# Kernel tuning notes

Hardware: AMD Instinct MI355X
Metric: run time of the kernel (lower is better)

The kernel has to match this reference:

```python
import jax, jax.numpy as jnp
import numpy as np

D_MODEL = 2048
N_HEADS = 16
D_K = D_MODEL // N_HEADS


def setup_inputs() -> dict:
    key = jax.random.key(0)
    k1, k2, k3 = jax.random.split(key, 3)
    x = jax.random.normal(k1, (2, 2048, D_MODEL), dtype=jnp.float32)
    # torch Linear convention: weight [out_features, in_features], y = x @ W.T
    W_qkv = jax.random.normal(k2, (3 * D_MODEL, D_MODEL), dtype=jnp.float32) * (D_MODEL ** -0.5)
    W_out = jax.random.normal(k3, (D_MODEL, D_MODEL), dtype=jnp.float32) * (D_MODEL ** -0.5)
    return {"x": x, "W_qkv": W_qkv, "W_out": W_out}


def reference(x, W_qkv, W_out):
    batch, seq_len, d_model = x.shape
    qkv = jnp.einsum('bsd,ed->bse', x, W_qkv)  # [B,S,3*D]
    qkv = qkv.reshape(batch, seq_len, 3, N_HEADS, D_K)
    qkv = jnp.transpose(qkv, (2, 0, 3, 1, 4))  # [3,B,H,S,Dk]
    Q, K, V = qkv[0], qkv[1], qkv[2]
    scores = jnp.einsum('bhqd,bhkd->bhqk', Q, K) / jnp.sqrt(jnp.float32(D_K))
    causal_mask = jnp.triu(jnp.ones((seq_len, seq_len), dtype=bool), k=1)
    scores = jnp.where(causal_mask, jnp.float32(-jnp.inf), scores)
    attn = jax.nn.softmax(scores, axis=-1)
    out = jnp.einsum('bhqk,bhkd->bhqd', attn, V)  # [B,H,S,Dk]
    out = jnp.transpose(out, (0, 2, 1, 3)).reshape(batch, seq_len, d_model)
    return jnp.einsum('bsd,ed->bse', out, W_out)
```

## Files before the change

### kernel.cpp

```cpp
#include <hip/hip_runtime.h>
#include <hip/hip_bf16.h>


typedef short bf16x8 __attribute__((ext_vector_type(8)));
typedef float f32x4  __attribute__((ext_vector_type(4)));

#define MFMA(a, b, c) __builtin_amdgcn_mfma_f32_16x16x32_bf16((a), (b), (c), 0, 0, 0)

#define GLDS16(gp, lp) __builtin_amdgcn_global_load_lds(                        \
    (const __attribute__((address_space(1))) void*)(gp),                        \
    (__attribute__((address_space(3))) void*)(lp), 16, 0, 0)

static __device__ __forceinline__ unsigned short f2bf(float f) {
    __hip_bfloat16 h = __float2bfloat16(f);
    return *reinterpret_cast<unsigned short*>(&h);
}

__global__ __launch_bounds__(256) void cvt3_f32_bf16(const float* __restrict__ x,
                                                     const float* __restrict__ wq,
                                                     const float* __restrict__ wo,
                                                     unsigned short* __restrict__ xb,
                                                     unsigned short* __restrict__ wqb,
                                                     unsigned short* __restrict__ wob) {
    const int i = blockIdx.x * 256 + threadIdx.x;
    const float* src; unsigned short* dst; int k;
    if (i < 2097152)      { src = x;  dst = xb;  k = i; }
    else if (i < 5242880) { src = wq; dst = wqb; k = i - 2097152; }
    else                  { src = wo; dst = wob; k = i - 5242880; }
    float4 v = reinterpret_cast<const float4*>(src)[k];
    ushort4 o;
    o.x = f2bf(v.x); o.y = f2bf(v.y); o.z = f2bf(v.z); o.w = f2bf(v.w);
    reinterpret_cast<ushort4*>(dst)[k] = o;
}

template <bool BF16OUT>
__global__ __launch_bounds__(256) void gemm_bt64(const unsigned short* __restrict__ A,
                                                 const unsigned short* __restrict__ W,
                                                 void* __restrict__ Cout,
                                                 int M, int N, int K) {
    __shared__ unsigned short As[128 * 64];
    __shared__ unsigned short Bs[128 * 64];
    const int tid = threadIdx.x;
    const int w = tid >> 6, lane = tid & 63;
    const int fr = lane & 15, fq = lane >> 4;
    const int m0 = blockIdx.y * 128, n0 = blockIdx.x * 128;
    const int wr = w >> 1, wc = w & 1;

    f32x4 acc[4][4];
#pragma unroll
    for (int a = 0; a < 4; a++)
#pragma unroll
        for (int b = 0; b < 4; b++) acc[a][b] = f32x4{0.f, 0.f, 0.f, 0.f};

    const int srow = lane >> 3;
    const int sce  = ((lane & 7) ^ (lane >> 3)) * 8;

    for (int kt = 0; kt < K; kt += 64) {
        __syncthreads();
#pragma unroll
        for (int q = 0; q < 4; ++q) {
            const int i = w * 4 + q;
            const int r = i * 8 + srow;
            GLDS16(A + (size_t)(m0 + r) * K + kt + sce, As + i * 512);
            GLDS16(W + (size_t)(n0 + r) * K + kt + sce, Bs + i * 512);
        }
        asm volatile("s_waitcnt vmcnt(0)" ::: "memory");
        __syncthreads();

#pragma unroll
        for (int kk = 0; kk < 2; ++kk) {
            bf16x8 af[4], bfr[4];
#pragma unroll
            for (int mi = 0; mi < 4; mi++) {
                const int row = wr * 64 + mi * 16 + fr;
                af[mi] = *reinterpret_cast<const bf16x8*>(
                    As + row * 64 + ((((kk * 64 + fq * 16) ^ ((fr & 7) << 4))) >> 1));
            }
#pragma unroll
            for (int ni = 0; ni < 4; ni++) {
                const int row = wc * 64 + ni * 16 + fr;
                bfr[ni] = *reinterpret_cast<const bf16x8*>(
                    Bs + row * 64 + ((((kk * 64 + fq * 16) ^ ((fr & 7) << 4))) >> 1));
            }
            __builtin_amdgcn_s_setprio(1);
#pragma unroll
            for (int mi = 0; mi < 4; mi++)
#pragma unroll
                for (int ni = 0; ni < 4; ni++)
                    acc[mi][ni] = MFMA(af[mi], bfr[ni], acc[mi][ni]);
            __builtin_amdgcn_s_setprio(0);
        }
    }

#pragma unroll
    for (int mi = 0; mi < 4; mi++) {
#pragma unroll
        for (int i = 0; i < 4; i++) {
            const int row = m0 + wr * 64 + mi * 16 + fq * 4 + i;
            const size_t base = (size_t)row * N + n0 + wc * 64 + fr;
#pragma unroll
            for (int ni = 0; ni < 4; ni++) {
                if (BF16OUT)
                    ((unsigned short*)Cout)[base + ni * 16] = f2bf(acc[mi][ni][i]);
                else
                    ((float*)Cout)[base + ni * 16] = acc[mi][ni][i];
            }
        }
    }
}

template <bool BF16OUT>
__global__ __launch_bounds__(256) void gemm_bt64_db(const unsigned short* __restrict__ A,
                                                    const unsigned short* __restrict__ W,
                                                    void* __restrict__ Cout,
                                                    int M, int N, int K) {
    __shared__ unsigned short As[2][128 * 64];
    __shared__ unsigned short Bs[2][128 * 64];
    const int tid = threadIdx.x;
    const int w = tid >> 6, lane = tid & 63;
    const int fr = lane & 15, fq = lane >> 4;
    const int m0 = blockIdx.y * 128, n0 = blockIdx.x * 128;
    const int wr = w >> 1, wc = w & 1;

    f32x4 acc[4][4];
#pragma unroll
    for (int a = 0; a < 4; a++)
#pragma unroll
        for (int b = 0; b < 4; b++) acc[a][b] = f32x4{0.f, 0.f, 0.f, 0.f};

    const int srow = lane >> 3;
    const int sce  = ((lane & 7) ^ (lane >> 3)) * 8;

    auto stage = [&](int kt, int bufi) {
#pragma unroll
        for (int q = 0; q < 4; ++q) {
            const int i = w * 4 + q;
            const int r = i * 8 + srow;
            GLDS16(A + (size_t)(m0 + r) * K + kt + sce, &As[bufi][i * 512]);
            GLDS16(W + (size_t)(n0 + r) * K + kt + sce, &Bs[bufi][i * 512]);
        }
    };

    const int NT = K >> 6;
    int cur = 0;
    stage(0, 0);
    __syncthreads();

    for (int it = 0; it < NT; ++it) {
        if (it + 1 < NT) stage((it + 1) << 6, cur ^ 1);
#pragma unroll
        for (int kk = 0; kk < 2; ++kk) {
            bf16x8 af[4], bfr[4];
#pragma unroll
            for (int mi = 0; mi < 4; mi++) {
                const int row = wr * 64 + mi * 16 + fr;
                af[mi] = *reinterpret_cast<const bf16x8*>(
                    &As[cur][0] + row * 64 + ((((kk * 64 + fq * 16) ^ ((fr & 7) << 4))) >> 1));
            }
#pragma unroll
            for (int ni = 0; ni < 4; ni++) {
                const int row = wc * 64 + ni * 16 + fr;
                bfr[ni] = *reinterpret_cast<const bf16x8*>(
                    &Bs[cur][0] + row * 64 + ((((kk * 64 + fq * 16) ^ ((fr & 7) << 4))) >> 1));
            }
            __builtin_amdgcn_s_setprio(1);
#pragma unroll
            for (int mi = 0; mi < 4; mi++)
#pragma unroll
                for (int ni = 0; ni < 4; ni++)
                    acc[mi][ni] = MFMA(af[mi], bfr[ni], acc[mi][ni]);
            __builtin_amdgcn_s_setprio(0);
        }
        __syncthreads();
        cur ^= 1;
    }

#pragma unroll
    for (int mi = 0; mi < 4; mi++) {
#pragma unroll
        for (int i = 0; i < 4; i++) {
            const int row = m0 + wr * 64 + mi * 16 + fq * 4 + i;
            const size_t base = (size_t)row * N + n0 + wc * 64 + fr;
#pragma unroll
            for (int ni = 0; ni < 4; ni++) {
                if (BF16OUT)
                    ((unsigned short*)Cout)[base + ni * 16] = f2bf(acc[mi][ni][i]);
                else
                    ((float*)Cout)[base + ni * 16] = acc[mi][ni][i];
            }
        }
    }
}

__global__ __launch_bounds__(256) void transpose_v(const unsigned short* __restrict__ qkv,
                                                   unsigned short* __restrict__ vT) {
    __shared__ unsigned short t[32][33];
    const int b = blockIdx.z, ts = blockIdx.x, tu = blockIdx.y;
    const int i = threadIdx.x >> 5, j = threadIdx.x & 31;
#pragma unroll
    for (int ii = 0; ii < 4; ++ii) {
        const int row = i + ii * 8;
        t[row][j] = qkv[(size_t)(b * 2048 + ts * 32 + row) * 6144 + 4096 + tu * 32 + j];
    }
    __syncthreads();
#pragma unroll
    for (int ii = 0; ii < 4; ++ii) {
        const int row = i + ii * 8;
        vT[(size_t)(b * 2048 + tu * 32 + row) * 2048 + ts * 32 + j] = t[j][row];
    }
}

#define SC2 (0.08838834764831845f * 1.4426950408889634f)
#define MREF 20.0f

__global__ __launch_bounds__(256, 2) void attn_fwd(const unsigned short* __restrict__ qkv,
                                                   const unsigned short* __restrict__ vT,
                                                   unsigned short* __restrict__ ao) {
    __shared__ __align__(16) char Kt[2][16384];
    __shared__ __align__(16) char Vt[2][16384];
    __shared__ __align__(16) unsigned short Ps[4][16 * 72];
    const int tid = threadIdx.x;
    const int w = tid >> 6, lane = tid & 63;
    const int fr = lane & 15, fq = lane >> 4;
    const int t = blockIdx.x;
    const int bh = t & 31;
    const int j = t >> 5;
    const int b = bh >> 4, h = bh & 15;

    const unsigned short* Qb = qkv + (size_t)b * 2048 * 6144 + h * 128;
    const unsigned short* Kb = qkv + (size_t)b * 2048 * 6144 + (16 + h) * 128;
    const unsigned short* Vb = vT + (size_t)bh * 128 * 2048;

    unsigned short* Pw = &Ps[w][0];
    const bf16x8 onesf = {0x3F80, 0x3F80, 0x3F80, 0x3F80, 0x3F80, 0x3F80, 0x3F80, 0x3F80};

    auto stage = [&](int kbs, int bufi) {
        const int k0s = kbs * 64;
        if (w < 2) {
#pragma unroll
            for (int q = 0; q < 8; ++q) {
                const int i = w * 8 + q;
                const int r = 4 * i + (lane >> 4);
                const int ce = ((((lane & 15) * 16) ^ ((r & 7) << 4))) >> 1;
                GLDS16(Kb + (size_t)(k0s + r) * 6144 + ce, &Kt[bufi][i * 1024]);
            }
        } else {
#pragma unroll
            for (int q = 0; q < 8; ++q) {
                const int i = (w - 2) * 8 + q;
                const int r = 8 * i + (lane >> 3);
                const int ce = ((lane & 7) ^ ((lane >> 3) & 7)) * 8;
                GLDS16(Vb + (size_t)r * 2048 + k0s + ce, &Vt[bufi][i * 1024]);
            }
        }
    };

#pragma unroll 1
    for (int seg = 0; seg < 2; ++seg) {
        const int g = seg ? j : 31 - j;
        const int q0 = g * 64 + w * 16;
        const int nb = g + 1;

        bf16x8 qf[4];
        {
            const unsigned short* qr = Qb + (size_t)(q0 + fr) * 6144 + fq * 8;
#pragma unroll
            for (int c = 0; c < 4; c++) qf[c] = *reinterpret_cast<const bf16x8*>(qr + c * 32);
        }

        f32x4 acc[8];
#pragma unroll
        for (int f = 0; f < 8; f++) acc[f] = f32x4{0.f, 0.f, 0.f, 0.f};
        f32x4 accL = f32x4{0.f, 0.f, 0.f, 0.f};

        int cur = 0;
        stage(0, 0);
        __syncthreads();

        for (int kb = 0; kb < nb; ++kb) {
            if (kb + 1 < nb) stage(kb + 1, cur ^ 1);
            const int k0 = kb * 64;
            const char* Kl = &Kt[cur][0];
            const char* Vl = &Vt[cur][0];

            f32x4 s[4];
#pragma unroll
            for (int th = 0; th < 2; ++th) {
                bf16x8 kf[2][4];
#pragma unroll
                for (int t2 = 0; t2 < 2; ++t2) {
                    const int tt = th * 2 + t2;
#pragma unroll
                    for (int c = 0; c < 4; ++c)
                        kf[t2][c] = *reinterpret_cast<const bf16x8*>(
                            Kl + (tt * 16 + fr) * 256 + ((c * 64 + fq * 16) ^ ((fr & 7) << 4)));
                }
                f32x4 a0 = f32x4{0.f, 0.f, 0.f, 0.f}, a1 = f32x4{0.f, 0.f, 0.f, 0.f};
                __builtin_amdgcn_s_setprio(1);
#pragma unroll
                for (int c = 0; c < 4; ++c) {
                    a0 = MFMA(qf[c], kf[0][c], a0);
                    a1 = MFMA(qf[c], kf[1][c], a1);
                }
                __builtin_amdgcn_s_setprio(0);
                s[th * 2] = a0; s[th * 2 + 1] = a1;
            }

            const bool diag = (kb == nb - 1);
#pragma unroll
            for (int i = 0; i < 4; ++i) {
                const int qrow = q0 + fq * 4 + i;
#pragma unroll
                for (int tt = 0; tt < 4; ++tt) {
                    float a = __builtin_fmaf(s[tt][i], SC2, -MREF);
                    if (diag && (k0 + tt * 16 + fr > qrow)) a = -__builtin_inff();
                    Pw[(fq * 4 + i) * 72 + tt * 16 + fr] = f2bf(exp2f(a));
                }
            }

#pragma unroll
            for (int h2 = 0; h2 < 2; ++h2) {
                bf16x8 pa = *reinterpret_cast<const bf16x8*>(Pw + fr * 72 + h2 * 32 + fq * 8);
                bf16x8 vf[8];
#pragma unroll
                for (int f = 0; f < 8; ++f)
                    vf[f] = *reinterpret_cast<const bf16x8*>(
                        Vl + (f * 16 + fr) * 128 + ((h2 * 64 + fq * 16) ^ ((fr & 7) << 4)));
                __builtin_amdgcn_s_setprio(1);
#pragma unroll
                for (int f = 0; f < 8; ++f) acc[f] = MFMA(pa, vf[f], acc[f]);
                accL = MFMA(pa, onesf, accL);
                __builtin_amdgcn_s_setprio(0);
            }

            __syncthreads();
            cur ^= 1;
        }

        float inv[4];
#pragma unroll
        for (int i = 0; i < 4; ++i) inv[i] = 1.0f / accL[i];
#pragma unroll
        for (int f = 0; f < 8; f++) {
#pragma unroll
            for (int i = 0; i < 4; i++) {
                const int qrow = q0 + fq * 4 + i;
                const float o = acc[f][i] * inv[i];
                ao[(size_t)(b * 2048 + qrow) * 2048 + h * 128 + f * 16 + fr] = f2bf(o);
            }
        }
    }
}

extern "C" void kernel_launch(void* const* d_in, const int* in_sizes, int n_in,
                              void* d_out, int out_size, void* d_ws, size_t ws_size,
                              hipStream_t stream) {
    const float* x    = (const float*)d_in[0];
    const float* Wqkv = (const float*)d_in[1];
    const float* Wout = (const float*)d_in[2];
    float* out = (float*)d_out;

    char* ws = (char*)d_ws;
    unsigned short* xb    = (unsigned short*)(ws);
    unsigned short* wqkvb = (unsigned short*)(ws + (size_t)(16 << 20));
    unsigned short* woutb = (unsigned short*)(ws + (size_t)(40 << 20));
    unsigned short* qkvb  = (unsigned short*)(ws + (size_t)(48 << 20));
    unsigned short* vTb   = (unsigned short*)(ws + (size_t)(16 << 20));
    unsigned short* attnb = (unsigned short*)(ws);

    cvt3_f32_bf16<<<24576, 256, 0, stream>>>(x, Wqkv, Wout, xb, wqkvb, woutb);

    gemm_bt64<true><<<dim3(48, 32), 256, 0, stream>>>(xb, wqkvb, qkvb, 4096, 6144, 2048);

    transpose_v<<<dim3(64, 64, 2), 256, 0, stream>>>(qkvb, vTb);

    attn_fwd<<<512, 256, 0, stream>>>(qkvb, vTb, attnb);

    gemm_bt64_db<false><<<dim3(16, 32), 256, 0, stream>>>(attnb, woutb, out, 4096, 2048, 2048);
}
```

Baseline: 242.2 us.

## Triple-buffer QKV GEMM with K=32 stages and async prefetch two ahead

Replaces the single-buffered QKV projection GEMM with a three-stage ring buffer using 32-wide K tiles. Global-to-LDS loads are issued two iterations ahead with a partial vmcnt wait, and only one barrier per iteration is used, so memory latency overlaps with the MFMA work. In exchange there are twice as many loop iterations with half the MFMAs per barrier, and the LDS swizzle is adapted for the narrower tile.

```diff
diff --git a/kernel.cpp b/kernel.cpp
--- a/kernel.cpp
+++ b/kernel.cpp
@@ -10,6 +10,8 @@
 #define GLDS16(gp, lp) __builtin_amdgcn_global_load_lds(                        \
     (const __attribute__((address_space(1))) void*)(gp),                        \
     (__attribute__((address_space(3))) void*)(lp), 16, 0, 0)
+
+#define FENCE asm volatile("" ::: "memory")
 
 static __device__ __forceinline__ unsigned short f2bf(float f) {
     __hip_bfloat16 h = __float2bfloat16(f);
@@ -33,13 +35,12 @@
     reinterpret_cast<ushort4*>(dst)[k] = o;
 }
 
-template <bool BF16OUT>
-__global__ __launch_bounds__(256) void gemm_bt64(const unsigned short* __restrict__ A,
-                                                 const unsigned short* __restrict__ W,
-                                                 void* __restrict__ Cout,
-                                                 int M, int N, int K) {
-    __shared__ unsigned short As[128 * 64];
-    __shared__ unsigned short Bs[128 * 64];
+__global__ __launch_bounds__(256) void gemm_qkv_r3(const unsigned short* __restrict__ A,
+                                                   const unsigned short* __restrict__ W,
+                                                   unsigned short* __restrict__ Cout,
+                                                   int M, int N, int K) {
+    __shared__ unsigned short As3[3][128 * 32];
+    __shared__ unsigned short Bs3[3][128 * 32];
     const int tid = threadIdx.x;
     const int w = tid >> 6, lane = tid & 63;
     const int fr = lane & 15, fq = lane >> 4;
@@ -52,44 +53,55 @@
 #pragma unroll
         for (int b = 0; b < 4; b++) acc[a][b] = f32x4{0.f, 0.f, 0.f, 0.f};
 
-    const int srow = lane >> 3;
-    const int sce  = ((lane & 7) ^ (lane >> 3)) * 8;
-
-    for (int kt = 0; kt < K; kt += 64) {
-        __syncthreads();
-#pragma unroll
-        for (int q = 0; q < 4; ++q) {
-            const int i = w * 4 + q;
-            const int r = i * 8 + srow;
-            GLDS16(A + (size_t)(m0 + r) * K + kt + sce, As + i * 512);
-            GLDS16(W + (size_t)(n0 + r) * K + kt + sce, Bs + i * 512);
-        }
-        asm volatile("s_waitcnt vmcnt(0)" ::: "memory");
-        __syncthreads();
-
-#pragma unroll
-        for (int kk = 0; kk < 2; ++kk) {
-            bf16x8 af[4], bfr[4];
-#pragma unroll
-            for (int mi = 0; mi < 4; mi++) {
-                const int row = wr * 64 + mi * 16 + fr;
-                af[mi] = *reinterpret_cast<const bf16x8*>(
-                    As + row * 64 + ((((kk * 64 + fq * 16) ^ ((fr & 7) << 4))) >> 1));
-            }
-#pragma unroll
-            for (int ni = 0; ni < 4; ni++) {
-                const int row = wc * 64 + ni * 16 + fr;
-                bfr[ni] = *reinterpret_cast<const bf16x8*>(
-                    Bs + row * 64 + ((((kk * 64 + fq * 16) ^ ((fr & 7) << 4))) >> 1));
-            }
-            __builtin_amdgcn_s_setprio(1);
-#pragma unroll
-            for (int mi = 0; mi < 4; mi++)
-#pragma unroll
-                for (int ni = 0; ni < 4; ni++)
-                    acc[mi][ni] = MFMA(af[mi], bfr[ni], acc[mi][ni]);
-            __builtin_amdgcn_s_setprio(0);
-        }
+    const int srow = lane >> 2;
+    const int sce  = ((lane & 3) ^ ((lane >> 3) & 3)) * 8;
+
+    auto stage = [&](int kt, int bufi) {
+#pragma unroll
+        for (int q = 0; q < 2; ++q) {
+            const int i = w * 2 + q;
+            const int r = i * 16 + srow;
+            GLDS16(A + (size_t)(m0 + r) * K + kt + sce, &As3[bufi][i * 512]);
+            GLDS16(W + (size_t)(n0 + r) * K + kt + sce, &Bs3[bufi][i * 512]);
+        }
+    };
+
+    const int NT = K >> 5;
+    stage(0, 0);
+    stage(32, 1);
+    int b0 = 0, b1 = 1, b2 = 2;
+
+#pragma unroll 1
+    for (int t = 0; t < NT; ++t) {
+        if (t + 1 < NT) { asm volatile("s_waitcnt vmcnt(4)" ::: "memory"); }
+        else            { asm volatile("s_waitcnt vmcnt(0)" ::: "memory"); }
+        FENCE; __builtin_amdgcn_s_barrier(); FENCE;
+        if (t + 2 < NT) stage((t + 2) << 5, b2);
+
+        const unsigned short* Ab = &As3[b0][0];
+        const unsigned short* Bb = &Bs3[b0][0];
+        bf16x8 af[4], bfr[4];
+#pragma unroll
+        for (int mi = 0; mi < 4; mi++) {
+            const int row = wr * 64 + mi * 16 + fr;
+            af[mi] = *reinterpret_cast<const bf16x8*>(
+                Ab + (row << 5) + (((fq << 3) ^ (((row >> 1) & 3) << 3))));
+        }
+#pragma unroll
+        for (int ni = 0; ni < 4; ni++) {
+            const int row = wc * 64 + ni * 16 + fr;
+            bfr[ni] = *reinterpret_cast<const bf16x8*>(
+                Bb + (row << 5) + (((fq << 3) ^ (((row >> 1) & 3) << 3))));
+        }
+        __builtin_amdgcn_s_setprio(1);
+#pragma unroll
+        for (int mi = 0; mi < 4; mi++)
+#pragma unroll
+            for (int ni = 0; ni < 4; ni++)
+                acc[mi][ni] = MFMA(af[mi], bfr[ni], acc[mi][ni]);
+        __builtin_amdgcn_s_setprio(0);
+
+        const int tmp = b0; b0 = b1; b1 = b2; b2 = tmp;
     }
 
 #pragma unroll
@@ -99,12 +111,8 @@
             const int row = m0 + wr * 64 + mi * 16 + fq * 4 + i;
             const size_t base = (size_t)row * N + n0 + wc * 64 + fr;
 #pragma unroll
-            for (int ni = 0; ni < 4; ni++) {
-                if (BF16OUT)
-                    ((unsigned short*)Cout)[base + ni * 16] = f2bf(acc[mi][ni][i]);
-                else
-                    ((float*)Cout)[base + ni * 16] = acc[mi][ni][i];
-            }
+            for (int ni = 0; ni < 4; ni++)
+                Cout[base + ni * 16] = f2bf(acc[mi][ni][i]);
         }
     }
 }
@@ -370,7 +378,7 @@
 
     cvt3_f32_bf16<<<24576, 256, 0, stream>>>(x, Wqkv, Wout, xb, wqkvb, woutb);
 
-    gemm_bt64<true><<<dim3(48, 32), 256, 0, stream>>>(xb, wqkvb, qkvb, 4096, 6144, 2048);
+    gemm_qkv_r3<<<dim3(48, 32), 256, 0, stream>>>(xb, wqkvb, qkvb, 4096, 6144, 2048);
 
     transpose_v<<<dim3(64, 64, 2), 256, 0, stream>>>(qkvb, vTb);
 
```

New measurement: 251.6 us. 1.04x slower.
